# Kernel tuning notes

Hardware: AMD Instinct MI355X
Metric: run time of the kernel (lower is better)

## Reference

```python
import jax, jax.numpy as jnp
import numpy as np
from jax import lax

B, T, INPUT, HIDDEN, OUT = 8192, 512, 10, 64, 1


def setup_inputs() -> dict:
    key = jax.random.key(0)
    k1, k2, k3, k4, k5 = jax.random.split(key, 5)
    padded_batch = jax.random.normal(k1, (B, T, INPUT), dtype=jnp.float32)
    lengths = jax.random.randint(k2, (B,), 1, T + 1, dtype=jnp.int64)
    # per-timestep distinct RNN weights, init scale 0.01 as in the torch module
    W_xh = jax.random.normal(k3, (T, INPUT, HIDDEN), dtype=jnp.float32) * 0.01
    W_hh = jax.random.normal(k4, (T, HIDDEN, HIDDEN), dtype=jnp.float32) * 0.01
    W_lin = jax.random.normal(k5, (HIDDEN, OUT), dtype=jnp.float32) * (1.0 / np.sqrt(HIDDEN))
    b_lin = jnp.zeros((OUT,), dtype=jnp.float32)
    return {"padded_batch": padded_batch, "lengths": lengths,
            "W_xh": W_xh, "W_hh": W_hh, "W_lin": W_lin, "b_lin": b_lin}


def reference(padded_batch, lengths, W_xh, W_hh, W_lin, b_lin):
    # padded_batch: [B, T, INPUT]; per-step weights W_xh: [T, INPUT, H], W_hh: [T, H, H]
    Bn = padded_batch.shape[0]
    x_tbd = jnp.swapaxes(padded_batch, 0, 1)  # [T, B, INPUT]
    t_idx = jnp.arange(T)

    def step(h, inputs):
        x_t, wxh, whh, t = inputs
        new_h = jnp.tanh(x_t @ wxh + h @ whh)          # [B, H]
        keep = (t < lengths)[:, None]                   # freeze samples past their length
        h = jnp.where(keep, new_h, h)
        return h, None

    h0 = jnp.zeros((Bn, HIDDEN), dtype=padded_batch.dtype)
    last_hidden, _ = lax.scan(step, h0, (x_tbd, W_xh, W_hh, t_idx))
    return last_hidden @ W_lin + b_lin  # [B, OUT]
```

## Files before the change

### kernel.cpp

```cpp
#include <hip/hip_runtime.h>
#include <stdint.h>

#define T_STEPS 512
#define HID     64
#define INP     10
#define MB      16
#define KS      88
#define HS      72
#define XS      40
#define WT_ELEMS (HID*KS)
#define WT_BYTES (WT_ELEMS*2)
#define WS_SLOTS (WT_BYTES/16)

typedef float  f32x4  __attribute__((ext_vector_type(4)));
typedef short  s16x8  __attribute__((ext_vector_type(8)));
typedef __bf16 bf16x8 __attribute__((ext_vector_type(8)));

__device__ __forceinline__ short f2bf(float f) {
    unsigned u = __builtin_bit_cast(unsigned, f);
    u = (u + 0x7FFFu + ((u >> 16) & 1u)) >> 16;
    return (short)u;
}
__device__ __forceinline__ float bf2f(short s) {
    unsigned u = ((unsigned)(unsigned short)s) << 16;
    return __builtin_bit_cast(float, u);
}

__global__ __launch_bounds__(256) void prep_w(const float* __restrict__ Wxh,
                                              const float* __restrict__ Whh,
                                              short* __restrict__ Wc) {
    __shared__ float s_hh[64 * 64];
    __shared__ float s_xh[INP * 64];
    const int t = blockIdx.x, tid = threadIdx.x;
    for (int i = tid; i < 64 * 64; i += 256) s_hh[i] = Whh[t * 4096 + i];
    for (int i = tid; i < INP * 64; i += 256) s_xh[i] = Wxh[t * (INP * 64) + i];
    __syncthreads();
    short* dst = Wc + (size_t)t * WT_ELEMS;
    for (int i = tid; i < WT_ELEMS; i += 256) {
        const int n = i / KS, k = i % KS;
        float v = 0.f;
        if (k < 64)      v = s_hh[k * 64 + n];
        else if (k < 74) v = s_xh[(k - 64) * 64 + n];
        dst[i] = f2bf(v);
    }
}

__global__ __launch_bounds__(256, 2) void rnn_main(const float* __restrict__ X,
                                                   const int* __restrict__ L,
                                                   const short* __restrict__ Wc,
                                                   const float* __restrict__ Wlin,
                                                   const float* __restrict__ blin,
                                                   float* __restrict__ out) {
    __shared__ __attribute__((aligned(16))) short Wb[2][WT_ELEMS + 16];
    __shared__ __attribute__((aligned(16))) short hb[2][MB * HS];
    __shared__ __attribute__((aligned(16))) short xb[2][MB * XS];
    __shared__ int len_s[MB];

    const int tid  = threadIdx.x;
    const int lane = tid & 63;
    const int wv   = tid >> 6;
    const int q    = lane >> 4;
    const int l    = lane & 15;
    const long long bbase = (long long)blockIdx.x * MB;

    for (int i = tid; i < MB * HS; i += 256) hb[0][i] = 0;
    for (int i = tid; i < MB * XS; i += 256) { xb[0][i] = 0; xb[1][i] = 0; }
    if (tid < 16) { Wb[0][WT_ELEMS + tid] = 0; Wb[1][WT_ELEMS + tid] = 0; }
    if (tid < MB) len_s[tid] = L[bbase + tid];
    __syncthreads();

    {
        const char* src = (const char*)(Wc);
        char* dst = (char*)&Wb[0][0];
#pragma unroll
        for (int i = 0; i < 3; ++i) {
            const int slot = tid + i * 256;
            if (slot < WS_SLOTS)
                __builtin_amdgcn_global_load_lds(
                    (const __attribute__((address_space(1))) unsigned int*)(src + slot * 16),
                    (__attribute__((address_space(3))) unsigned int*)(dst + slot * 16),
                    16, 0, 0);
        }
    }
    const int xs = tid / INP, xi = tid % INP;
    float xreg = 0.f;
    if (tid < MB * INP) {
        xb[0][xs * XS + xi] = f2bf(X[(bbase + xs) * (T_STEPS * INP) + 0 * INP + xi]);
        xreg = X[(bbase + xs) * (T_STEPS * INP) + 1 * INP + xi];
    }
    __syncthreads();

    float hc[4] = {0.f, 0.f, 0.f, 0.f};
    int len4[4];
#pragma unroll
    for (int r = 0; r < 4; ++r) len4[r] = len_s[q * 4 + r];
    const int colw = wv * 16 + l;

    for (int t = 0; t < T_STEPS; ++t) {
        const int cur = t & 1, nxt = cur ^ 1;

        if (t + 1 < T_STEPS) {
            const char* src = (const char*)(Wc) + (size_t)(t + 1) * WT_BYTES;
            char* dst = (char*)&Wb[nxt][0];
#pragma unroll
            for (int i = 0; i < 3; ++i) {
                const int slot = tid + i * 256;
                if (slot < WS_SLOTS)
                    __builtin_amdgcn_global_load_lds(
                        (const __attribute__((address_space(1))) unsigned int*)(src + slot * 16),
                        (__attribute__((address_space(3))) unsigned int*)(dst + slot * 16),
                        16, 0, 0);
            }
        }

        if (tid < MB * INP) {
            xb[nxt][xs * XS + xi] = f2bf(xreg);
            if (t + 2 < T_STEPS)
                xreg = X[(bbase + xs) * (T_STEPS * INP) + (long long)(t + 2) * INP + xi];
        }

        const s16x8 a0 = *(const s16x8*)&hb[cur][l * HS + q * 8];
        const s16x8 a1 = *(const s16x8*)&hb[cur][l * HS + 32 + q * 8];
        const s16x8 a2 = *(const s16x8*)&xb[cur][l * XS + q * 8];
        const s16x8 b0 = *(const s16x8*)&Wb[cur][colw * KS + q * 8];
        const s16x8 b1 = *(const s16x8*)&Wb[cur][colw * KS + 32 + q * 8];
        const s16x8 b2 = *(const s16x8*)&Wb[cur][colw * KS + 64 + q * 8];

        f32x4 z = {0.f, 0.f, 0.f, 0.f};
        f32x4 acc0 = __builtin_amdgcn_mfma_f32_16x16x32_bf16(
                  __builtin_bit_cast(bf16x8, a0), __builtin_bit_cast(bf16x8, b0), z, 0, 0, 0);
        f32x4 acc1 = __builtin_amdgcn_mfma_f32_16x16x32_bf16(
                  __builtin_bit_cast(bf16x8, a1), __builtin_bit_cast(bf16x8, b1), z, 0, 0, 0);
        f32x4 acc2 = __builtin_amdgcn_mfma_f32_16x16x32_bf16(
                  __builtin_bit_cast(bf16x8, a2), __builtin_bit_cast(bf16x8, b2), z, 0, 0, 0);

#pragma unroll
        for (int r = 0; r < 4; ++r) {
            const float a  = acc0[r] + acc1[r] + acc2[r];
            const float e  = __expf(2.f * a);
            const float th = 1.f - 2.f * __builtin_amdgcn_rcpf(e + 1.f);
            hc[r] = (t < len4[r]) ? th : hc[r];
            hb[nxt][(q * 4 + r) * HS + colw] = f2bf(hc[r]);
        }
        __syncthreads();
    }

    const float wl = Wlin[lane];
    const float bl = blin[0];
#pragma unroll
    for (int it = 0; it < 4; ++it) {
        const int s = wv + it * 4;
        float v = bf2f(hb[0][s * HS + lane]) * wl;
#pragma unroll
        for (int off = 32; off > 0; off >>= 1) v += __shfl_down(v, off);
        if (lane == 0) out[bbase + s] = v + bl;
    }
}

extern "C" void kernel_launch(void* const* d_in, const int* in_sizes, int n_in,
                              void* d_out, int out_size, void* d_ws, size_t ws_size,
                              hipStream_t stream) {
    const float* X    = (const float*)d_in[0];
    const int*   L    = (const int*)d_in[1];
    const float* Wxh  = (const float*)d_in[2];
    const float* Whh  = (const float*)d_in[3];
    const float* Wlin = (const float*)d_in[4];
    const float* blin = (const float*)d_in[5];
    float*       out  = (float*)d_out;
    short*       Wc   = (short*)d_ws;

    prep_w<<<T_STEPS, 256, 0, stream>>>(Wxh, Whh, Wc);
    rnn_main<<<8192 / MB, 256, 0, stream>>>(X, L, Wc, Wlin, blin, out);
}
```

Before: 589.7 us.

## Deepen weight and input prefetch pipeline with async LDS loads and relaxed waits

Weight tiles move to a triple-buffered LDS ring that is prefetched two steps ahead. Input rows are now loaded asynchronously into a four-deep LDS staging buffer through global_load_lds instead of per-thread register loads. The per-step __syncthreads is replaced by explicit vmcnt/lgkmcnt waits plus s_barrier, so only older loads are waited on and the global-load latency stays off the recurrence's critical path. Smaller changes pad the prep_w shared arrays to avoid bank conflicts and use the hardware bf16 conversion. The trade-offs are more LDS use, which may affect the two-blocks-per-CU occupancy, and fragile hand-tuned waitcnt counts.

```diff
diff --git a/kernel.cpp b/kernel.cpp
--- a/kernel.cpp
+++ b/kernel.cpp
@@ -11,16 +11,24 @@
 #define WT_ELEMS (HID*KS)
 #define WT_BYTES (WT_ELEMS*2)
 #define WS_SLOTS (WT_BYTES/16)
+#define WB_SLOTS 768
+#define WB_ELEMS (WB_SLOTS*8)
 
 typedef float  f32x4  __attribute__((ext_vector_type(4)));
 typedef short  s16x8  __attribute__((ext_vector_type(8)));
 typedef __bf16 bf16x8 __attribute__((ext_vector_type(8)));
+
+typedef const __attribute__((address_space(1))) unsigned int* gp_t;
+typedef __attribute__((address_space(3))) unsigned int*       lp_t;
 
 __device__ __forceinline__ short f2bf(float f) {
     unsigned u = __builtin_bit_cast(unsigned, f);
     u = (u + 0x7FFFu + ((u >> 16) & 1u)) >> 16;
     return (short)u;
 }
+__device__ __forceinline__ short f2bfh(float f) {
+    return __builtin_bit_cast(short, (__bf16)f);
+}
 __device__ __forceinline__ float bf2f(short s) {
     unsigned u = ((unsigned)(unsigned short)s) << 16;
     return __builtin_bit_cast(float, u);
@@ -29,18 +37,20 @@
 __global__ __launch_bounds__(256) void prep_w(const float* __restrict__ Wxh,
                                               const float* __restrict__ Whh,
                                               short* __restrict__ Wc) {
-    __shared__ float s_hh[64 * 64];
-    __shared__ float s_xh[INP * 64];
+    __shared__ float s_hh[64 * 65];
+    __shared__ float s_xh[INP * 65];
     const int t = blockIdx.x, tid = threadIdx.x;
-    for (int i = tid; i < 64 * 64; i += 256) s_hh[i] = Whh[t * 4096 + i];
-    for (int i = tid; i < INP * 64; i += 256) s_xh[i] = Wxh[t * (INP * 64) + i];
+    for (int i = tid; i < 64 * 64; i += 256)
+        s_hh[(i >> 6) * 65 + (i & 63)] = Whh[t * 4096 + i];
+    for (int i = tid; i < INP * 64; i += 256)
+        s_xh[(i >> 6) * 65 + (i & 63)] = Wxh[t * (INP * 64) + i];
     __syncthreads();
     short* dst = Wc + (size_t)t * WT_ELEMS;
     for (int i = tid; i < WT_ELEMS; i += 256) {
         const int n = i / KS, k = i % KS;
         float v = 0.f;
-        if (k < 64)      v = s_hh[k * 64 + n];
-        else if (k < 74) v = s_xh[(k - 64) * 64 + n];
+        if (k < 64)      v = s_hh[k * 65 + n];
+        else if (k < 74) v = s_xh[(k - 64) * 65 + n];
         dst[i] = f2bf(v);
     }
 }
@@ -51,9 +61,10 @@
                                                    const float* __restrict__ Wlin,
                                                    const float* __restrict__ blin,
                                                    float* __restrict__ out) {
-    __shared__ __attribute__((aligned(16))) short Wb[2][WT_ELEMS + 16];
+    __shared__ __attribute__((aligned(16))) short Wb[3][WB_ELEMS];
     __shared__ __attribute__((aligned(16))) short hb[2][MB * HS];
     __shared__ __attribute__((aligned(16))) short xb[2][MB * XS];
+    __shared__ __attribute__((aligned(16))) float xf[4][256];
     __shared__ int len_s[MB];
 
     const int tid  = threadIdx.x;
@@ -63,68 +74,77 @@
     const int l    = lane & 15;
     const long long bbase = (long long)blockIdx.x * MB;
 
+    const int ws2_src = (((tid + 512) < WS_SLOTS) ? (tid + 512) : 0) * 16;
+    auto issue_w = [&](int tp, int buf) {
+        const char* src = (const char*)Wc + (size_t)tp * WT_BYTES;
+        char* dst = (char*)&Wb[buf][0];
+        __builtin_amdgcn_global_load_lds((gp_t)(src + tid * 16),
+                                         (lp_t)(dst + tid * 16), 16, 0, 0);
+        __builtin_amdgcn_global_load_lds((gp_t)(src + (tid + 256) * 16),
+                                         (lp_t)(dst + (tid + 256) * 16), 16, 0, 0);
+        __builtin_amdgcn_global_load_lds((gp_t)(src + ws2_src),
+                                         (lp_t)(dst + (tid + 512) * 16), 16, 0, 0);
+    };
+
+    const int s47   = (lane < 48) ? lane : 47;
+    const int xrow  = s47 / 3;
+    const int xpart = s47 - xrow * 3;
+    const int xpoff = (xpart == 0) ? 0 : ((xpart == 1) ? 8 : 24);
+    const char* xsrc0 = (const char*)X + (size_t)(bbase + xrow) * (T_STEPS * INP * 4) + xpoff;
+    auto issue_xf = [&](int tx, int buf) {
+        __builtin_amdgcn_global_load_lds((gp_t)(xsrc0 + (size_t)tx * (INP * 4)),
+                                         (lp_t)((char*)&xf[buf][0] + lane * 16), 16, 0, 0);
+    };
+
+    const int xs = tid / INP, xi = tid % INP;
+    const int xfoff = xs * 48 + xi * 4 + (xi < 4 ? 0 : 8);
+
+    if (tid < MB) len_s[tid] = L[bbase + tid];
     for (int i = tid; i < MB * HS; i += 256) hb[0][i] = 0;
     for (int i = tid; i < MB * XS; i += 256) { xb[0][i] = 0; xb[1][i] = 0; }
-    if (tid < 16) { Wb[0][WT_ELEMS + tid] = 0; Wb[1][WT_ELEMS + tid] = 0; }
-    if (tid < MB) len_s[tid] = L[bbase + tid];
-    __syncthreads();
-
-    {
-        const char* src = (const char*)(Wc);
-        char* dst = (char*)&Wb[0][0];
-#pragma unroll
-        for (int i = 0; i < 3; ++i) {
-            const int slot = tid + i * 256;
-            if (slot < WS_SLOTS)
-                __builtin_amdgcn_global_load_lds(
-                    (const __attribute__((address_space(1))) unsigned int*)(src + slot * 16),
-                    (__attribute__((address_space(3))) unsigned int*)(dst + slot * 16),
-                    16, 0, 0);
-        }
-    }
-    const int xs = tid / INP, xi = tid % INP;
-    float xreg = 0.f;
+
+    issue_w(0, 0);
+    issue_xf(0, 0);
+    issue_xf(1, 1);
+    issue_w(1, 1);
+    issue_xf(2, 2);
+    asm volatile("s_waitcnt vmcnt(4)" ::: "memory");
+    __builtin_amdgcn_sched_barrier(0);
     if (tid < MB * INP) {
-        xb[0][xs * XS + xi] = f2bf(X[(bbase + xs) * (T_STEPS * INP) + 0 * INP + xi]);
-        xreg = X[(bbase + xs) * (T_STEPS * INP) + 1 * INP + xi];
-    }
-    __syncthreads();
+        const float x0 = *(const float*)((const char*)&xf[0][0] + xfoff);
+        xb[0][xs * XS + xi] = f2bfh(x0);
+    }
+    asm volatile("s_waitcnt lgkmcnt(0)" ::: "memory");
+    __builtin_amdgcn_s_barrier();
 
     float hc[4] = {0.f, 0.f, 0.f, 0.f};
     int len4[4];
 #pragma unroll
     for (int r = 0; r < 4; ++r) len4[r] = len_s[q * 4 + r];
     const int colw = wv * 16 + l;
+    const int woff = colw * KS + q * 8;
+
+    int rb = 0;
 
     for (int t = 0; t < T_STEPS; ++t) {
         const int cur = t & 1, nxt = cur ^ 1;
-
-        if (t + 1 < T_STEPS) {
-            const char* src = (const char*)(Wc) + (size_t)(t + 1) * WT_BYTES;
-            char* dst = (char*)&Wb[nxt][0];
-#pragma unroll
-            for (int i = 0; i < 3; ++i) {
-                const int slot = tid + i * 256;
-                if (slot < WS_SLOTS)
-                    __builtin_amdgcn_global_load_lds(
-                        (const __attribute__((address_space(1))) unsigned int*)(src + slot * 16),
-                        (__attribute__((address_space(3))) unsigned int*)(dst + slot * 16),
-                        16, 0, 0);
-            }
+        const int pb  = (rb >= 1) ? rb - 1 : 2;
+
+        const int tpw = (t + 2 < T_STEPS) ? t + 2 : T_STEPS - 1;
+        const int tpx = (t + 3 < T_STEPS) ? t + 3 : T_STEPS - 1;
+        issue_w(tpw, pb);
+        issue_xf(tpx, (t + 3) & 3);
+
+        if (tid < MB * INP) {
+            const float xv = *(const float*)((const char*)&xf[(t + 1) & 3][0] + xfoff);
+            xb[nxt][xs * XS + xi] = f2bfh(xv);
         }
-
-        if (tid < MB * INP) {
-            xb[nxt][xs * XS + xi] = f2bf(xreg);
-            if (t + 2 < T_STEPS)
-                xreg = X[(bbase + xs) * (T_STEPS * INP) + (long long)(t + 2) * INP + xi];
-        }
-
         const s16x8 a0 = *(const s16x8*)&hb[cur][l * HS + q * 8];
         const s16x8 a1 = *(const s16x8*)&hb[cur][l * HS + 32 + q * 8];
         const s16x8 a2 = *(const s16x8*)&xb[cur][l * XS + q * 8];
-        const s16x8 b0 = *(const s16x8*)&Wb[cur][colw * KS + q * 8];
-        const s16x8 b1 = *(const s16x8*)&Wb[cur][colw * KS + 32 + q * 8];
-        const s16x8 b2 = *(const s16x8*)&Wb[cur][colw * KS + 64 + q * 8];
+        const s16x8 b0 = *(const s16x8*)&Wb[rb][woff];
+        const s16x8 b1 = *(const s16x8*)&Wb[rb][woff + 32];
+        const s16x8 b2 = *(const s16x8*)&Wb[rb][woff + 64];
 
         f32x4 z = {0.f, 0.f, 0.f, 0.f};
         f32x4 acc0 = __builtin_amdgcn_mfma_f32_16x16x32_bf16(
@@ -140,10 +160,17 @@
             const float e  = __expf(2.f * a);
             const float th = 1.f - 2.f * __builtin_amdgcn_rcpf(e + 1.f);
             hc[r] = (t < len4[r]) ? th : hc[r];
-            hb[nxt][(q * 4 + r) * HS + colw] = f2bf(hc[r]);
+            hb[nxt][(q * 4 + r) * HS + colw] = f2bfh(hc[r]);
         }
-        __syncthreads();
-    }
+
+        asm volatile("s_waitcnt vmcnt(4)");
+        asm volatile("s_waitcnt lgkmcnt(0)" ::: "memory");
+        __builtin_amdgcn_s_barrier();
+
+        rb = (rb == 2) ? 0 : rb + 1;
+    }
+
+    asm volatile("s_waitcnt vmcnt(0)" ::: "memory");
 
     const float wl = Wlin[lane];
     const float bl = blin[0];
```

Result: slower. 637.1 us (+8.0%).
